# Kernel optimization log

Measured on AMD Instinct MI355X. Metric: run time of the kernel, lower is better.

## Reference

```python
import jax, jax.numpy as jnp
import numpy as np

ADMP = 16  # admp_channel -> K = ADMP*ADMP keypoints


def setup_inputs() -> dict:
    key = jax.random.key(0)
    kA, kB = jax.random.split(key)
    B, C, H, W = 4, 512, 128, 128
    feature_A = jax.random.normal(kA, (B, C, H, W), dtype=jnp.float32)
    feature_B = jax.random.normal(kB, (B, C, H, W), dtype=jnp.float32)
    return {"feature_A": feature_A, "feature_B": feature_B}


def _forward(feature_A, feature_B):
    B, C, H, W = feature_A.shape
    S = ADMP
    bh, bw = H // S, W // S  # uniform adaptive-pool windows (H,W divisible by S)
    K = S * S
    HW = H * W

    # featureSelect: channel-sum response, adaptive max pool with indices
    resp = feature_A.sum(1)  # [B,H,W]
    blocks = resp.reshape(B, S, bh, S, bw).transpose(0, 1, 3, 2, 4).reshape(B, K, bh * bw)
    loc = jnp.argmax(blocks, axis=-1)  # [B,K] index within window (row-major)
    k = jnp.arange(K)
    bi, bj = k // S, k % S  # window grid coords
    row_A = bi[None, :] * bh + loc // bw  # [B,K]
    col_A = bj[None, :] * bw + loc % bw
    idx = row_A * W + col_A  # flat indices into H*W

    # gather keypoint descriptors from feature_A
    fa_flat = feature_A.reshape(B, C, HW)
    desc = jnp.take_along_axis(fa_flat, idx[:, None, :], axis=2)  # [B,C,K]

    # squared L2 distance of every descriptor vs every feature_B position
    fb_flat = feature_B.reshape(B, C, HW)
    cross = jnp.einsum('bck,bcn->bkn', desc, fb_flat)  # [B,K,HW]
    dn = (desc ** 2).sum(1)  # [B,K]
    bn = (fb_flat ** 2).sum(1)  # [B,HW]
    dist = dn[:, :, None] - 2.0 * cross + bn[:, None, :]  # [B,K,HW]

    min_idx = jnp.argmin(dist, axis=-1)  # [B,K]
    min_vals = jnp.min(dist, axis=-1)    # [B,K] (min_value_T)

    row_B = min_idx // W
    col_B = min_idx % W
    drow = row_A - row_B  # = -(row_B - row_A)
    dcol = col_A - col_B

    # getTranslationalOffsetByMode: most frequent (drow,dcol) pair per batch;
    # tie broken by first occurrence (matches Python dict insertion + stable sort)
    code = drow * (4 * W) + dcol  # unique encoding, |dcol| < 2W
    counts = (code[:, :, None] == code[:, None, :]).sum(-1)  # [B,K]
    best = jnp.argmax(counts, axis=-1)  # [B]
    dx = jnp.take_along_axis(drow, best[:, None], axis=1)[:, 0]
    dy = jnp.take_along_axis(dcol, best[:, None], axis=1)[:, 0]
    offsets = jnp.stack([dx, dy], axis=-1).astype(jnp.int32)  # [B,2]
    return offsets, min_vals


def reference(feature_A, feature_B):
    offsets, min_vals = _forward(feature_A, feature_B)
    return offsets, min_vals
```

## Files before the change

kernel.cpp:

```cpp
#include <hip/hip_runtime.h>
#include <stdint.h>

#define BDIM 4
#define CDIM 512
#define HDIM 128
#define WDIM 128
#define HWDIM (HDIM*WDIM)
#define SADMP 16
#define BHW 8
#define KKP 256

using short8 = __attribute__((ext_vector_type(8))) short;
using f32x4  = __attribute__((ext_vector_type(4))) float;

__device__ __forceinline__ unsigned short f2bf(float f) {
    unsigned u = __float_as_uint(f);
    unsigned r = (u + 0x7fffu + ((u >> 16) & 1u)) >> 16;
    return (unsigned short)r;
}
__device__ __forceinline__ float bf2f(unsigned short h) {
    return __uint_as_float(((unsigned)h) << 16);
}
__device__ __forceinline__ unsigned int ordf(float f) {
    unsigned u = __float_as_uint(f);
    return (u & 0x80000000u) ? ~u : (u | 0x80000000u);
}
__device__ __forceinline__ void step_barrier() {
    asm volatile("s_waitcnt lgkmcnt(0)" ::: "memory");
    __builtin_amdgcn_s_barrier();
}

__global__ void resp_part_kernel(const float* __restrict__ A, float* __restrict__ part) {
    int gid = blockIdx.x * blockDim.x + threadIdx.x;
    int hw = gid & (HWDIM - 1);
    int rest = gid >> 14;
    int b = rest >> 3, cq = rest & 7;
    const float* p = A + (size_t)b * CDIM * HWDIM + (size_t)(cq * 64) * HWDIM + hw;
    float s0 = 0.f, s1 = 0.f, s2 = 0.f, s3 = 0.f;
    #pragma unroll 4
    for (int c = 0; c < 64; c += 4) {
        s0 += p[(size_t)(c + 0) * HWDIM];
        s1 += p[(size_t)(c + 1) * HWDIM];
        s2 += p[(size_t)(c + 2) * HWDIM];
        s3 += p[(size_t)(c + 3) * HWDIM];
    }
    part[gid] = (s0 + s1) + (s2 + s3);
}
__global__ void resp_comb_kernel(const float* __restrict__ part, float* __restrict__ resp) {
    int gid = blockIdx.x * blockDim.x + threadIdx.x;
    int hw = gid & (HWDIM - 1);
    int b = gid >> 14;
    const float* p = part + (size_t)(b * 8) * HWDIM + hw;
    float s = 0.f;
    #pragma unroll
    for (int cq = 0; cq < 8; cq++) s += p[(size_t)cq * HWDIM];
    resp[gid] = s;
}

__global__ void argmax_kernel(const float* __restrict__ resp, int* __restrict__ kp) {
    int win = blockIdx.x;
    int b = win / KKP, k = win % KKP;
    int bi = k / SADMP, bj = k % SADMP;
    int l = threadIdx.x;
    int r = l >> 3, c = l & 7;
    int h = bi * BHW + r, w = bj * BHW + c;
    float v = resp[b * HWDIM + h * WDIM + w];
    int idx = l;
    #pragma unroll
    for (int off = 32; off; off >>= 1) {
        float ov = __shfl_down(v, off);
        int   oi = __shfl_down(idx, off);
        if (ov > v || (ov == v && oi < idx)) { v = ov; idx = oi; }
    }
    if (l == 0) {
        int row = bi * BHW + (idx >> 3);
        int col = bj * BHW + (idx & 7);
        kp[win] = row * WDIM + col;
    }
}

__global__ void convert_kernel(const float* __restrict__ A, const int* __restrict__ kp,
                               uint4* __restrict__ frag, float* __restrict__ dn) {
    int blk = blockIdx.x;
    int b = blk >> 4, mf = blk & 15;
    int t = threadIdx.x;
    int l = t & 63, q0 = t >> 6;
    int ml = l & 15;
    int m  = mf * 16 + ml;
    int cg = (l >> 4) * 8;
    int idx = kp[b * KKP + m];
    const float* Ab = A + (size_t)b * CDIM * HWDIM + idx;
    float sq = 0.f;
    #pragma unroll
    for (int qq = 0; qq < 4; qq++) {
        int q = q0 * 4 + qq;
        unsigned hi[4], lo[4];
        #pragma unroll
        for (int jj = 0; jj < 4; jj++) {
            int c0 = q * 32 + cg + jj * 2;
            float v0 = Ab[(size_t)c0 * HWDIM];
            float v1 = Ab[(size_t)(c0 + 1) * HWDIM];
            sq = fmaf(v0, v0, sq);
            sq = fmaf(v1, v1, sq);
            unsigned short h0 = f2bf(v0), h1 = f2bf(v1);
            unsigned short g0 = f2bf(v0 - bf2f(h0)), g1 = f2bf(v1 - bf2f(h1));
            hi[jj] = (unsigned)h0 | ((unsigned)h1 << 16);
            lo[jj] = (unsigned)g0 | ((unsigned)g1 << 16);
        }
        frag[((size_t)b * 2 + 0) * 16384 + mf * 1024 + q * 64 + l] = make_uint4(hi[0], hi[1], hi[2], hi[3]);
        frag[((size_t)b * 2 + 1) * 16384 + mf * 1024 + q * 64 + l] = make_uint4(lo[0], lo[1], lo[2], lo[3]);
    }
    __shared__ float red[16][17];
    red[ml][(l >> 4) * 4 + q0] = sq;
    __syncthreads();
    if (t < 16) {
        float s = 0.f;
        #pragma unroll
        for (int i = 0; i < 16; i++) s += red[t][i];
        dn[b * KKP + mf * 16 + t] = s;
    }
}

__global__ __launch_bounds__(512) void dist_mfma_kernel(
    const uint4* __restrict__ fragA, const float* __restrict__ fb,
    const float* __restrict__ dn, unsigned long long* __restrict__ minkey)
{
    const int n0 = blockIdx.x * 64;
    const int b  = blockIdx.y;
    const int t  = threadIdx.x;
    const int l  = t & 63;
    const int w  = t >> 6;

    __shared__ char sb[2][16384];
    __shared__ float bnp[8][64];
    __shared__ float bnf[64];
    __shared__ float dnl[256];

    if (t < 256) dnl[t] = dn[b * KKP + t];

    f32x4 acc[2][4] = {};

    const int scol = t & 63;
    const int sw   = t >> 6;
    const int wbase = ((sw >> 2) << 12) + ((scol >> 4) << 10) + (((((sw & 3) << 4) + (scol & 15))) << 4);
    const float* fbp = fb + (size_t)b * CDIM * HWDIM + (size_t)(sw * 8) * HWDIM + n0 + scol;
    float bnacc = 0.f;

    const short8* fA = (const short8*)fragA;
    const size_t a0Hi = ((size_t)b * 2 + 0) * 16384 + (size_t)(w * 2 + 0) * 1024 + l;
    const size_t a1Hi = ((size_t)b * 2 + 0) * 16384 + (size_t)(w * 2 + 1) * 1024 + l;
    const size_t a0Lo = ((size_t)b * 2 + 1) * 16384 + (size_t)(w * 2 + 0) * 1024 + l;
    const size_t a1Lo = ((size_t)b * 2 + 1) * 16384 + (size_t)(w * 2 + 1) * 1024 + l;

    float v[8];
    #pragma unroll
    for (int i = 0; i < 8; i++) v[i] = fbp[(size_t)i * HWDIM];
    {
        unsigned hi[4], lo[4];
        #pragma unroll
        for (int jj = 0; jj < 4; jj++) {
            float v0 = v[jj * 2], v1 = v[jj * 2 + 1];
            bnacc = fmaf(v0, v0, bnacc);
            bnacc = fmaf(v1, v1, bnacc);
            unsigned short h0 = f2bf(v0), h1 = f2bf(v1);
            unsigned short g0 = f2bf(v0 - bf2f(h0)), g1 = f2bf(v1 - bf2f(h1));
            hi[jj] = (unsigned)h0 | ((unsigned)h1 << 16);
            lo[jj] = (unsigned)g0 | ((unsigned)g1 << 16);
        }
        *(uint4*)(&sb[0][wbase])        = make_uint4(hi[0], hi[1], hi[2], hi[3]);
        *(uint4*)(&sb[0][wbase + 8192]) = make_uint4(lo[0], lo[1], lo[2], lo[3]);
    }
    #pragma unroll
    for (int i = 0; i < 8; i++) v[i] = fbp[(size_t)(64 + i) * HWDIM];
    short8 aA0 = fA[a0Hi], aA1 = fA[a1Hi], aA2 = fA[a0Lo], aA3 = fA[a1Lo];
    step_barrier();

    for (int s = 0; s < 8; s++) {
        const int cur = s & 1;
        const char* rb = sb[cur];

        const size_t qB = (size_t)(s * 2 + 1) * 64;
        short8 aB0 = fA[a0Hi + qB];
        short8 aB1 = fA[a1Hi + qB];
        short8 aB2 = fA[a0Lo + qB];
        short8 aB3 = fA[a1Lo + qB];

        {
            const char* rp = rb + l * 16;
            #pragma unroll
            for (int nf = 0; nf < 4; nf++) {
                short8 bh = *(const short8*)(rp + nf * 1024);
                short8 bl = *(const short8*)(rp + nf * 1024 + 8192);
                acc[0][nf] = __builtin_amdgcn_mfma_f32_16x16x32_bf16(aA0, bh, acc[0][nf], 0, 0, 0);
                acc[0][nf] = __builtin_amdgcn_mfma_f32_16x16x32_bf16(aA0, bl, acc[0][nf], 0, 0, 0);
                acc[0][nf] = __builtin_amdgcn_mfma_f32_16x16x32_bf16(aA2, bh, acc[0][nf], 0, 0, 0);
                acc[1][nf] = __builtin_amdgcn_mfma_f32_16x16x32_bf16(aA1, bh, acc[1][nf], 0, 0, 0);
                acc[1][nf] = __builtin_amdgcn_mfma_f32_16x16x32_bf16(aA1, bl, acc[1][nf], 0, 0, 0);
                acc[1][nf] = __builtin_amdgcn_mfma_f32_16x16x32_bf16(aA3, bh, acc[1][nf], 0, 0, 0);
            }
        }

        if (s < 7) {
            unsigned hi[4], lo[4];
            #pragma unroll
            for (int jj = 0; jj < 4; jj++) {
                float v0 = v[jj * 2], v1 = v[jj * 2 + 1];
                bnacc = fmaf(v0, v0, bnacc);
                bnacc = fmaf(v1, v1, bnacc);
                unsigned short h0 = f2bf(v0), h1 = f2bf(v1);
                unsigned short g0 = f2bf(v0 - bf2f(h0)), g1 = f2bf(v1 - bf2f(h1));
                hi[jj] = (unsigned)h0 | ((unsigned)h1 << 16);
                lo[jj] = (unsigned)g0 | ((unsigned)g1 << 16);
            }
            char* wp = (char*)sb[cur ^ 1] + wbase;
            *(uint4*)(wp)        = make_uint4(hi[0], hi[1], hi[2], hi[3]);
            *(uint4*)(wp + 8192) = make_uint4(lo[0], lo[1], lo[2], lo[3]);
            if (s < 6) {
                #pragma unroll
                for (int i = 0; i < 8; i++)
                    v[i] = fbp[(size_t)((s + 2) * 64 + i) * HWDIM];
            }
        }

        if (s < 7) {
            const size_t qN = (size_t)(s * 2 + 2) * 64;
            aA0 = fA[a0Hi + qN];
            aA1 = fA[a1Hi + qN];
            aA2 = fA[a0Lo + qN];
            aA3 = fA[a1Lo + qN];
        }

        {
            const char* rp = rb + 4096 + l * 16;
            #pragma unroll
            for (int nf = 0; nf < 4; nf++) {
                short8 bh = *(const short8*)(rp + nf * 1024);
                short8 bl = *(const short8*)(rp + nf * 1024 + 8192);
                acc[0][nf] = __builtin_amdgcn_mfma_f32_16x16x32_bf16(aB0, bh, acc[0][nf], 0, 0, 0);
                acc[0][nf] = __builtin_amdgcn_mfma_f32_16x16x32_bf16(aB0, bl, acc[0][nf], 0, 0, 0);
                acc[0][nf] = __builtin_amdgcn_mfma_f32_16x16x32_bf16(aB2, bh, acc[0][nf], 0, 0, 0);
                acc[1][nf] = __builtin_amdgcn_mfma_f32_16x16x32_bf16(aB1, bh, acc[1][nf], 0, 0, 0);
                acc[1][nf] = __builtin_amdgcn_mfma_f32_16x16x32_bf16(aB1, bl, acc[1][nf], 0, 0, 0);
                acc[1][nf] = __builtin_amdgcn_mfma_f32_16x16x32_bf16(aB3, bh, acc[1][nf], 0, 0, 0);
            }
        }

        if (s < 7) step_barrier();
    }

    bnp[sw][scol] = bnacc;
    __syncthreads();
    if (t < 64) {
        float s = 0.f;
        #pragma unroll
        for (int i = 0; i < 8; i++) s += bnp[i][t];
        bnf[t] = s;
    }
    __syncthreads();

    #pragma unroll
    for (int mfl = 0; mfl < 2; mfl++) {
        #pragma unroll
        for (int r = 0; r < 4; r++) {
            int m = w * 32 + mfl * 16 + (l >> 4) * 4 + r;
            float dnm = dnl[m];
            unsigned long long best = ~0ull;
            #pragma unroll
            for (int nf = 0; nf < 4; nf++) {
                int nloc = nf * 16 + (l & 15);
                float d = dnm - 2.f * acc[mfl][nf][r] + bnf[nloc];
                unsigned long long key = ((unsigned long long)ordf(d) << 32) | (unsigned)(n0 + nloc);
                if (key < best) best = key;
            }
            #pragma unroll
            for (int off = 1; off < 16; off <<= 1) {
                unsigned long long o = __shfl_xor(best, off);
                if (o < best) best = o;
            }
            if ((l & 15) == 0) atomicMin(&minkey[b * KKP + m], best);
        }
    }
}

__global__ void finalize_kernel(const unsigned long long* __restrict__ minkey,
                                const int* __restrict__ kp,
                                float* __restrict__ out)
{
    int b = blockIdx.x;
    int k = threadIdx.x;
    unsigned long long key = minkey[b * KKP + k];
    unsigned n   = (unsigned)(key & 0xffffffffu);
    unsigned top = (unsigned)(key >> 32);
    unsigned fbits = (top & 0x80000000u) ? (top ^ 0x80000000u) : ~top;
    out[8 + b * KKP + k] = __uint_as_float(fbits);

    int idxA = kp[b * KKP + k];
    int rowA = idxA >> 7, colA = idxA & 127;
    int rowB = (int)(n >> 7), colB = (int)(n & 127);
    int drow = rowA - rowB, dcol = colA - colB;
    int code = (drow + 256) * 1024 + (dcol + 256);

    __shared__ int codes[KKP];
    __shared__ int keys[KKP];
    codes[k] = code;
    __syncthreads();
    int cnt = 0;
    for (int j = 0; j < KKP; j++) cnt += (codes[j] == code);
    keys[k] = cnt * 256 + (255 - k);
    __syncthreads();
    for (int s = 128; s; s >>= 1) {
        if (k < s) keys[k] = max(keys[k], keys[k + s]);
        __syncthreads();
    }
    if (k == 0) {
        int bestk = 255 - (keys[0] & 255);
        int bc = codes[bestk];
        int dr = bc / 1024 - 256, dc = bc % 1024 - 256;
        out[b * 2 + 0] = (float)dr;
        out[b * 2 + 1] = (float)dc;
    }
}

extern "C" void kernel_launch(void* const* d_in, const int* in_sizes, int n_in,
                              void* d_out, int out_size, void* d_ws, size_t ws_size,
                              hipStream_t stream) {
    const float* A  = (const float*)d_in[0];
    const float* Bf = (const float*)d_in[1];
    float* out = (float*)d_out;
    char* ws = (char*)d_ws;

    float* resp = (float*)ws;
    int*   kp   = (int*)(ws + 262144);
    float* dn   = (float*)(ws + 266240);
    unsigned long long* minkey = (unsigned long long*)(ws + 270336);
    uint4* frag = (uint4*)(ws + 278528);
    float* part = (float*)(ws + 278528 + 2097152);

    hipMemsetAsync(minkey, 0xFF, BDIM * KKP * sizeof(unsigned long long), stream);
    resp_part_kernel<<<BDIM * 8 * HWDIM / 256, 256, 0, stream>>>(A, part);
    resp_comb_kernel<<<BDIM * HWDIM / 256, 256, 0, stream>>>(part, resp);
    argmax_kernel<<<BDIM * KKP, 64, 0, stream>>>(resp, kp);
    convert_kernel<<<BDIM * 16, 256, 0, stream>>>(A, kp, frag, dn);
    dist_mfma_kernel<<<dim3(256, BDIM), 512, 0, stream>>>(frag, Bf, dn, minkey);
    finalize_kernel<<<BDIM, KKP, 0, stream>>>(minkey, kp, out);
}
```

Before: 136.0 us.

## Reorder dist kernel loop to issue global loads before MFMAs, remap blocks

Inside the distance MFMA main loop, the bf16 conversion and LDS store of the next feature_B chunk, plus the loads of both halves of the A fragments, now run before one merged block of MFMAs. The MFMA block is wrapped in s_setprio. Global load latency should then overlap a longer MFMA run instead of splitting it. The grid is also flattened to 1D with a remap of (u&7)*128+(u>>3), which spreads consecutive blocks across batches/XCDs. Costs are higher register pressure from holding the next A fragments, and possible cache-locality changes from the remap.

New measurement: 117.6 us. 13.5% less time.

```diff
diff --git a/kernel.cpp b/kernel.cpp
--- a/kernel.cpp
+++ b/kernel.cpp
@@ -125,8 +125,11 @@
     const uint4* __restrict__ fragA, const float* __restrict__ fb,
     const float* __restrict__ dn, unsigned long long* __restrict__ minkey)
 {
-    const int n0 = blockIdx.x * 64;
-    const int b  = blockIdx.y;
+    const int u    = blockIdx.x;
+    const int g    = (u & 7) * 128 + (u >> 3);
+    const int b    = g >> 8;
+    const int n0   = (g & 255) * 64;
+
     const int t  = threadIdx.x;
     const int l  = t & 63;
     const int w  = t >> 6;
@@ -179,27 +182,6 @@
         const int cur = s & 1;
         const char* rb = sb[cur];
 
-        const size_t qB = (size_t)(s * 2 + 1) * 64;
-        short8 aB0 = fA[a0Hi + qB];
-        short8 aB1 = fA[a1Hi + qB];
-        short8 aB2 = fA[a0Lo + qB];
-        short8 aB3 = fA[a1Lo + qB];
-
-        {
-            const char* rp = rb + l * 16;
-            #pragma unroll
-            for (int nf = 0; nf < 4; nf++) {
-                short8 bh = *(const short8*)(rp + nf * 1024);
-                short8 bl = *(const short8*)(rp + nf * 1024 + 8192);
-                acc[0][nf] = __builtin_amdgcn_mfma_f32_16x16x32_bf16(aA0, bh, acc[0][nf], 0, 0, 0);
-                acc[0][nf] = __builtin_amdgcn_mfma_f32_16x16x32_bf16(aA0, bl, acc[0][nf], 0, 0, 0);
-                acc[0][nf] = __builtin_amdgcn_mfma_f32_16x16x32_bf16(aA2, bh, acc[0][nf], 0, 0, 0);
-                acc[1][nf] = __builtin_amdgcn_mfma_f32_16x16x32_bf16(aA1, bh, acc[1][nf], 0, 0, 0);
-                acc[1][nf] = __builtin_amdgcn_mfma_f32_16x16x32_bf16(aA1, bl, acc[1][nf], 0, 0, 0);
-                acc[1][nf] = __builtin_amdgcn_mfma_f32_16x16x32_bf16(aA3, bh, acc[1][nf], 0, 0, 0);
-            }
-        }
-
         if (s < 7) {
             unsigned hi[4], lo[4];
             #pragma unroll
@@ -222,20 +204,40 @@
             }
         }
 
+        const size_t qB = (size_t)(s * 2 + 1) * 64;
+        short8 aB0 = fA[a0Hi + qB];
+        short8 aB1 = fA[a1Hi + qB];
+        short8 aB2 = fA[a0Lo + qB];
+        short8 aB3 = fA[a1Lo + qB];
+
+        short8 aN0 = aA0, aN1 = aA1, aN2 = aA2, aN3 = aA3;
         if (s < 7) {
             const size_t qN = (size_t)(s * 2 + 2) * 64;
-            aA0 = fA[a0Hi + qN];
-            aA1 = fA[a1Hi + qN];
-            aA2 = fA[a0Lo + qN];
-            aA3 = fA[a1Lo + qN];
+            aN0 = fA[a0Hi + qN];
+            aN1 = fA[a1Hi + qN];
+            aN2 = fA[a0Lo + qN];
+            aN3 = fA[a1Lo + qN];
         }
 
         {
-            const char* rp = rb + 4096 + l * 16;
+            const char* rp0 = rb + l * 16;
+            const char* rp1 = rb + 4096 + l * 16;
+            __builtin_amdgcn_s_setprio(1);
             #pragma unroll
             for (int nf = 0; nf < 4; nf++) {
-                short8 bh = *(const short8*)(rp + nf * 1024);
-                short8 bl = *(const short8*)(rp + nf * 1024 + 8192);
+                short8 bh = *(const short8*)(rp0 + nf * 1024);
+                short8 bl = *(const short8*)(rp0 + nf * 1024 + 8192);
+                acc[0][nf] = __builtin_amdgcn_mfma_f32_16x16x32_bf16(aA0, bh, acc[0][nf], 0, 0, 0);
+                acc[0][nf] = __builtin_amdgcn_mfma_f32_16x16x32_bf16(aA0, bl, acc[0][nf], 0, 0, 0);
+                acc[0][nf] = __builtin_amdgcn_mfma_f32_16x16x32_bf16(aA2, bh, acc[0][nf], 0, 0, 0);
+                acc[1][nf] = __builtin_amdgcn_mfma_f32_16x16x32_bf16(aA1, bh, acc[1][nf], 0, 0, 0);
+                acc[1][nf] = __builtin_amdgcn_mfma_f32_16x16x32_bf16(aA1, bl, acc[1][nf], 0, 0, 0);
+                acc[1][nf] = __builtin_amdgcn_mfma_f32_16x16x32_bf16(aA3, bh, acc[1][nf], 0, 0, 0);
+            }
+            #pragma unroll
+            for (int nf = 0; nf < 4; nf++) {
+                short8 bh = *(const short8*)(rp1 + nf * 1024);
+                short8 bl = *(const short8*)(rp1 + nf * 1024 + 8192);
                 acc[0][nf] = __builtin_amdgcn_mfma_f32_16x16x32_bf16(aB0, bh, acc[0][nf], 0, 0, 0);
                 acc[0][nf] = __builtin_amdgcn_mfma_f32_16x16x32_bf16(aB0, bl, acc[0][nf], 0, 0, 0);
                 acc[0][nf] = __builtin_amdgcn_mfma_f32_16x16x32_bf16(aB2, bh, acc[0][nf], 0, 0, 0);
@@ -243,8 +245,10 @@
                 acc[1][nf] = __builtin_amdgcn_mfma_f32_16x16x32_bf16(aB1, bl, acc[1][nf], 0, 0, 0);
                 acc[1][nf] = __builtin_amdgcn_mfma_f32_16x16x32_bf16(aB3, bh, acc[1][nf], 0, 0, 0);
             }
-        }
-
+            __builtin_amdgcn_s_setprio(0);
+        }
+
+        aA0 = aN0; aA1 = aN1; aA2 = aN2; aA3 = aN3;
         if (s < 7) step_barrier();
     }
 
@@ -341,6 +345,6 @@
     resp_comb_kernel<<<BDIM * HWDIM / 256, 256, 0, stream>>>(part, resp);
     argmax_kernel<<<BDIM * KKP, 64, 0, stream>>>(resp, kp);
     convert_kernel<<<BDIM * 16, 256, 0, stream>>>(A, kp, frag, dn);
-    dist_mfma_kernel<<<dim3(256, BDIM), 512, 0, stream>>>(frag, Bf, dn, minkey);
+    dist_mfma_kernel<<<1024, 512, 0, stream>>>(frag, Bf, dn, minkey);
     finalize_kernel<<<BDIM, KKP, 0, stream>>>(minkey, kp, out);
 }
```
